# Kernel tuning notes

Hardware: AMD Instinct MI355X
Metric: run time of the kernel (lower is better)

The kernel has to match this reference:

```python
import jax, jax.numpy as jnp
import numpy as np

B, N, D_POINTS, D_MODEL = 2, 2048, 32, 512


def _gather(feat, idx):
    # feat: [B, N, C], idx: [B, N, K] -> [B, N, K, C]
    return jax.vmap(lambda f, i: f[i])(feat, idx)


def setup_inputs() -> dict:
    key = jax.random.key(0)
    ks = jax.random.split(key, 20)
    def lin(k, fan_in, fan_out):
        bound = 1.0 / np.sqrt(fan_in)
        return jax.random.uniform(k, (fan_in, fan_out), jnp.float32, -bound, bound)
    def bias(k, fan_in, fan_out):
        bound = 1.0 / np.sqrt(fan_in)
        return jax.random.uniform(k, (fan_out,), jnp.float32, -bound, bound)
    return {
        "xyz": jax.random.normal(ks[0], (B, N, 3), jnp.float32),
        "points": jax.random.normal(ks[1], (B, N, D_POINTS), jnp.float32),
        "fc1_w": lin(ks[2], D_POINTS, D_MODEL), "fc1_b": bias(ks[3], D_POINTS, D_MODEL),
        "fc2_w": lin(ks[4], D_MODEL, D_POINTS), "fc2_b": bias(ks[5], D_MODEL, D_POINTS),
        "delta_w1": lin(ks[6], 3, D_MODEL), "delta_b1": bias(ks[7], 3, D_MODEL),
        "delta_w2": lin(ks[8], D_MODEL, D_MODEL), "delta_b2": bias(ks[9], D_MODEL, D_MODEL),
        "gamma_w1": lin(ks[10], D_MODEL, D_MODEL), "gamma_b1": bias(ks[11], D_MODEL, D_MODEL),
        "gamma_w2": lin(ks[12], D_MODEL, D_MODEL), "gamma_b2": bias(ks[13], D_MODEL, D_MODEL),
        "wq": lin(ks[14], D_MODEL, D_MODEL),
        "wk": lin(ks[15], D_MODEL, D_MODEL),
        "wv": lin(ks[16], D_MODEL, D_MODEL),
        "knn_k": 16,
    }


def reference(xyz, points, fc1_w, fc1_b, fc2_w, fc2_b,
              delta_w1, delta_b1, delta_w2, delta_b2,
              gamma_w1, gamma_b1, gamma_w2, gamma_b2,
              wq, wk, wv, knn_k):
    # square_distance: [B, N, N]
    sq = jnp.sum(xyz * xyz, axis=-1)
    dists = sq[:, :, None] + sq[:, None, :] - 2.0 * jnp.einsum('bnc,bmc->bnm', xyz, xyz)
    # knn: k smallest distances (argsort[:, :, :k] equivalent)
    _, knn_idx = jax.lax.top_k(-dists, knn_k)           # [B, N, K]
    knn_xyz = _gather(xyz, knn_idx)                      # [B, N, K, 3]

    pre = points
    x = points @ fc1_w + fc1_b                           # [B, N, d_model]
    q = x @ wq                                           # [B, N, d_model]
    k = _gather(x @ wk, knn_idx)                         # [B, N, K, d_model]
    v = _gather(x @ wv, knn_idx)                         # [B, N, K, d_model]

    # positional encoding MLP on delta xyz
    delta = xyz[:, :, None, :] - knn_xyz                 # [B, N, K, 3]
    pos_enc = jax.nn.relu(delta @ delta_w1 + delta_b1) @ delta_w2 + delta_b2

    # gamma MLP on (q - k + pos_enc)
    a = q[:, :, None, :] - k + pos_enc
    a = jax.nn.relu(a @ gamma_w1 + gamma_b1) @ gamma_w2 + gamma_b2

    scale = jnp.asarray(np.sqrt(D_MODEL), a.dtype)
    attn = jax.nn.softmax(a / scale, axis=-2)            # softmax over neighbors, per channel

    res = jnp.sum(attn * (v + pos_enc), axis=2)          # einsum 'bmnf,bmnf->bmf'
    res = res @ fc2_w + fc2_b + pre                      # [B, N, d_points]
    return res, attn
```

## Files before the change

### kernel.cpp

```cpp
#include <hip/hip_runtime.h>
#include <hip/hip_bf16.h>
#include <math.h>

typedef __bf16 bf16_t;
typedef float f32x4 __attribute__((ext_vector_type(4)));
typedef bf16_t bf16x8 __attribute__((ext_vector_type(8)));

#define BM 128
#define BN 128
#define BKT 64
#define LDK 72

struct TC6 { const float* src[6]; bf16_t* dst[6]; };
__global__ __launch_bounds__(256) void tcast6_kernel(TC6 tc) {
  int job = blockIdx.x >> 10;
  int idx = (blockIdx.x & 1023) * 256 + threadIdx.x;
  int n = idx >> 9, k = idx & 511;
  tc.dst[job][idx] = (bf16_t)tc.src[job][k * 512 + n];
}

__global__ __launch_bounds__(256) void knn_kernel(const float* __restrict__ xyz, int* __restrict__ knn) {
  __shared__ float sx[2048], sy[2048], sz[2048], sq[2048];
  int tid = threadIdx.x;
  int lane = tid & 63, wave = tid >> 6;
  int gq = blockIdx.x * 4 + wave;
  int b  = gq >> 11;
  int base = b << 11;
  for (int p = tid; p < 2048; p += 256) {
    float x = xyz[(base + p) * 3 + 0];
    float y = xyz[(base + p) * 3 + 1];
    float z = xyz[(base + p) * 3 + 2];
    sx[p] = x; sy[p] = y; sz[p] = z;
    sq[p] = __fadd_rn(__fadd_rn(__fmul_rn(x, x), __fmul_rn(y, y)), __fmul_rn(z, z));
  }
  __syncthreads();
  int iq = gq & 2047;
  float qx = sx[iq], qy = sy[iq], qz = sz[iq], sqi = sq[iq];

  unsigned long long key[32];
  #pragma unroll
  for (int j = 0; j < 32; ++j) {
    int p = lane + j * 64;
    float d = __fmul_rn(sx[p], qx);
    d = fmaf(sy[p], qy, d);
    d = fmaf(sz[p], qz, d);
    float dist = __fsub_rn(__fadd_rn(sqi, sq[p]), __fmul_rn(2.0f, d));
    unsigned int bits = __float_as_uint(dist);
    unsigned int sk = bits ^ (unsigned int)(((int)bits >> 31) | 0x80000000);
    key[j] = ((unsigned long long)sk << 32) | (unsigned int)p;
  }

  int r = 0;
  #pragma unroll 1
  for (int s = 0; s < 16; ++s) {
    unsigned long long m = key[0];
    #pragma unroll
    for (int j = 1; j < 32; ++j) m = (key[j] < m) ? key[j] : m;
    #pragma unroll
    for (int off = 32; off > 0; off >>= 1) {
      unsigned long long o = (unsigned long long)__shfl_xor((long long)m, off);
      if (o < m) m = o;
    }
    if (lane == s) r = base + (int)(m & 0xFFFFFFFFu);
    #pragma unroll
    for (int j = 0; j < 32; ++j) key[j] = (key[j] == m) ? ~0ULL : key[j];
  }
  if (lane < 16) knn[gq * 16 + lane] = r;
}

__global__ __launch_bounds__(256) void xfeat_kernel(const float* __restrict__ points, const float* __restrict__ fc1_w,
                                                    const float* __restrict__ fc1_b, bf16_t* __restrict__ xb) {
  __shared__ float p[32];
  int m = blockIdx.x, tid = threadIdx.x;
  if (tid < 32) p[tid] = points[m * 32 + tid];
  __syncthreads();
  for (int c = tid; c < 512; c += 256) {
    float a = fc1_b[c];
    #pragma unroll
    for (int kk = 0; kk < 32; ++kk) a = fmaf(p[kk], fc1_w[kk * 512 + c], a);
    xb[m * 512 + c] = (bf16_t)a;
  }
}

__global__ __launch_bounds__(256) void h1_kernel(const float* __restrict__ xyz, const int* __restrict__ knn,
                                                 const float* __restrict__ dw1, const float* __restrict__ db1,
                                                 bf16_t* __restrict__ h1) {
  __shared__ float w0[512], w1r[512], w2[512], bb[512];
  int g = blockIdx.x, tid = threadIdx.x;
  for (int c = tid; c < 512; c += 256) {
    w0[c] = dw1[c]; w1r[c] = dw1[512 + c]; w2[c] = dw1[1024 + c]; bb[c] = db1[c];
  }
  float xi0 = xyz[g * 3 + 0], xi1 = xyz[g * 3 + 1], xi2 = xyz[g * 3 + 2];
  __syncthreads();
  for (int slot = 0; slot < 16; ++slot) {
    int j = knn[g * 16 + slot];
    float d0 = xi0 - xyz[j * 3 + 0];
    float d1 = xi1 - xyz[j * 3 + 1];
    float d2 = xi2 - xyz[j * 3 + 2];
    int m = g * 16 + slot;
    for (int c = tid; c < 512; c += 256) {
      float h = fmaf(d2, w2[c], fmaf(d1, w1r[c], d0 * w0[c])) + bb[c];
      h1[m * 512 + c] = (bf16_t)fmaxf(h, 0.0f);
    }
  }
}

__global__ __launch_bounds__(256) void final_kernel(const float* __restrict__ res_mid, const float* __restrict__ fc2_w,
                                                    const float* __restrict__ fc2_b, const float* __restrict__ points,
                                                    float* __restrict__ out) {
  int oid = blockIdx.x * 256 + threadIdx.x;
  int m = oid >> 5, c = oid & 31;
  float a = fc2_b[c];
  const float* rm = res_mid + m * 512;
  for (int kk = 0; kk < 512; ++kk) a = fmaf(rm[kk], fc2_w[kk * 32 + c], a);
  out[oid] = a + points[oid];
}

template <int SRC, int EPI>
__global__ __launch_bounds__(256) void gemm_kernel(
    const bf16_t* __restrict__ A, const bf16_t* __restrict__ Bt,
    float* __restrict__ Cf, bf16_t* __restrict__ Cb,
    const float* __restrict__ bias, int ldc,
    const float* __restrict__ qkv, float* pe_attn,
    const int* __restrict__ knn, float* __restrict__ res_mid)
{
  __shared__ bf16_t Alds[BM][LDK];
  __shared__ bf16_t Blds[BN][LDK];
  int tid  = threadIdx.x;
  int lane = tid & 63, wave = tid >> 6;
  int wr = wave >> 1, wc = wave & 1;
  int lr = lane & 15, lg = lane >> 4;
  int n0 = blockIdx.x * BN, m0 = blockIdx.y * BM;

  f32x4 acc[4][4];
  #pragma unroll
  for (int i = 0; i < 4; ++i)
    #pragma unroll
    for (int j = 0; j < 4; ++j) acc[i][j] = (f32x4){0.f, 0.f, 0.f, 0.f};

  int srow = tid >> 3;
  int sc8  = (tid & 7) * 8;

  for (int k0 = 0; k0 < 512; k0 += BKT) {
    #pragma unroll
    for (int it = 0; it < 4; ++it) {
      int r = srow + it * 32;
      if (SRC == 0) {
        bf16x8 v = *(const bf16x8*)(A + (size_t)(m0 + r) * 512 + k0 + sc8);
        *(bf16x8*)(&Alds[r][sc8]) = v;
      } else {
        int m = m0 + r;
        int g = m >> 4;
        int j = knn[m];
        const float* qp = qkv + (size_t)g * 1536 + k0 + sc8;
        const float* kp = qkv + (size_t)j * 1536 + 512 + k0 + sc8;
        const float* pp = pe_attn + (size_t)m * 512 + k0 + sc8;
        f32x4 q0 = *(const f32x4*)qp,       q1 = *(const f32x4*)(qp + 4);
        f32x4 k0v = *(const f32x4*)kp,      k1v = *(const f32x4*)(kp + 4);
        f32x4 p0 = *(const f32x4*)pp,       p1 = *(const f32x4*)(pp + 4);
        bf16x8 o;
        #pragma unroll
        for (int u = 0; u < 4; ++u) o[u] = (bf16_t)(q0[u] - k0v[u] + p0[u]);
        #pragma unroll
        for (int u = 0; u < 4; ++u) o[4 + u] = (bf16_t)(q1[u] - k1v[u] + p1[u]);
        *(bf16x8*)(&Alds[r][sc8]) = o;
      }
      bf16x8 vb = *(const bf16x8*)(Bt + (size_t)(n0 + r) * 512 + k0 + sc8);
      *(bf16x8*)(&Blds[r][sc8]) = vb;
    }
    __syncthreads();
    #pragma unroll
    for (int kk = 0; kk < BKT; kk += 32) {
      int ko = kk + 8 * lg;
      bf16x8 af[4], bfr[4];
      #pragma unroll
      for (int mi = 0; mi < 4; ++mi) af[mi] = *(const bf16x8*)(&Alds[wr * 64 + mi * 16 + lr][ko]);
      #pragma unroll
      for (int nj = 0; nj < 4; ++nj) bfr[nj] = *(const bf16x8*)(&Blds[wc * 64 + nj * 16 + lr][ko]);
      #pragma unroll
      for (int mi = 0; mi < 4; ++mi)
        #pragma unroll
        for (int nj = 0; nj < 4; ++nj)
          acc[mi][nj] = __builtin_amdgcn_mfma_f32_16x16x32_bf16(af[mi], bfr[nj], acc[mi][nj], 0, 0, 0);
    }
    __syncthreads();
  }

  if (EPI == 0 || EPI == 1) {
    #pragma unroll
    for (int mi = 0; mi < 4; ++mi)
      #pragma unroll
      for (int nj = 0; nj < 4; ++nj) {
        int col = n0 + wc * 64 + nj * 16 + lr;
        #pragma unroll
        for (int r = 0; r < 4; ++r) {
          int row = m0 + wr * 64 + mi * 16 + lg * 4 + r;
          float v = acc[mi][nj][r];
          if (EPI == 1) v += bias[col];
          Cf[(size_t)row * ldc + col] = v;
        }
      }
  } else if (EPI == 2) {
    #pragma unroll
    for (int mi = 0; mi < 4; ++mi)
      #pragma unroll
      for (int nj = 0; nj < 4; ++nj) {
        int col = n0 + wc * 64 + nj * 16 + lr;
        #pragma unroll
        for (int r = 0; r < 4; ++r) {
          int row = m0 + wr * 64 + mi * 16 + lg * 4 + r;
          Cb[(size_t)row * ldc + col] = (bf16_t)fmaxf(acc[mi][nj][r] + bias[col], 0.0f);
        }
      }
  } else {
    const float scale = 22.62741699796952f;
    #pragma unroll
    for (int mi = 0; mi < 4; ++mi) {
      int g = (m0 + wr * 64 + mi * 16) >> 4;
      #pragma unroll
      for (int nj = 0; nj < 4; ++nj) {
        int col = n0 + wc * 64 + nj * 16 + lr;
        float sv[4];
        float mx = -INFINITY;
        #pragma unroll
        for (int r = 0; r < 4; ++r) {
          sv[r] = (acc[mi][nj][r] + bias[col]) / scale;
          mx = fmaxf(mx, sv[r]);
        }
        mx = fmaxf(mx, __shfl_xor(mx, 16));
        mx = fmaxf(mx, __shfl_xor(mx, 32));
        float e[4], sum = 0.f;
        #pragma unroll
        for (int r = 0; r < 4; ++r) { e[r] = expf(sv[r] - mx); sum += e[r]; }
        sum += __shfl_xor(sum, 16);
        sum += __shfl_xor(sum, 32);
        float part = 0.f;
        #pragma unroll
        for (int r = 0; r < 4; ++r) {
          int row = g * 16 + lg * 4 + r;
          float at = e[r] / sum;
          int j = knn[row];
          float vv  = qkv[(size_t)j * 1536 + 1024 + col];
          float pev = pe_attn[(size_t)row * 512 + col];
          part = fmaf(at, vv + pev, part);
          pe_attn[(size_t)row * 512 + col] = at;
        }
        part += __shfl_xor(part, 16);
        part += __shfl_xor(part, 32);
        if (lg == 0) res_mid[(size_t)g * 512 + col] = part;
      }
    }
  }
}

extern "C" void kernel_launch(void* const* d_in, const int* in_sizes, int n_in,
                              void* d_out, int out_size, void* d_ws, size_t ws_size,
                              hipStream_t stream) {
  const float* xyz    = (const float*)d_in[0];
  const float* points = (const float*)d_in[1];
  const float* fc1_w  = (const float*)d_in[2];
  const float* fc1_b  = (const float*)d_in[3];
  const float* fc2_w  = (const float*)d_in[4];
  const float* fc2_b  = (const float*)d_in[5];
  const float* dw1    = (const float*)d_in[6];
  const float* db1    = (const float*)d_in[7];
  const float* dw2    = (const float*)d_in[8];
  const float* db2    = (const float*)d_in[9];
  const float* gw1    = (const float*)d_in[10];
  const float* gb1    = (const float*)d_in[11];
  const float* gw2    = (const float*)d_in[12];
  const float* gb2    = (const float*)d_in[13];
  const float* wq     = (const float*)d_in[14];
  const float* wk     = (const float*)d_in[15];
  const float* wv     = (const float*)d_in[16];

  float* out = (float*)d_out;
  float* attn_pe = out + 131072;

  char* w = (char*)d_ws;
  bf16_t* wqkvT  = (bf16_t*)w; w += (size_t)1536 * 512 * 2;
  bf16_t* dw2T   = (bf16_t*)w; w += (size_t)512 * 512 * 2;
  bf16_t* gw1T   = (bf16_t*)w; w += (size_t)512 * 512 * 2;
  bf16_t* gw2T   = (bf16_t*)w; w += (size_t)512 * 512 * 2;
  int*    knn    = (int*)w;    w += (size_t)65536 * 4;
  bf16_t* xb     = (bf16_t*)w; w += (size_t)4096 * 512 * 2;
  float*  qkv    = (float*)w;  w += (size_t)4096 * 1536 * 4;
  bf16_t* h12    = (bf16_t*)w; w += (size_t)65536 * 512 * 2;
  float*  res_mid= (float*)w;  w += (size_t)4096 * 512 * 4;

  TC6 tc;
  tc.src[0] = wq;  tc.dst[0] = wqkvT;
  tc.src[1] = wk;  tc.dst[1] = wqkvT + 512 * 512;
  tc.src[2] = wv;  tc.dst[2] = wqkvT + 2 * 512 * 512;
  tc.src[3] = dw2; tc.dst[3] = dw2T;
  tc.src[4] = gw1; tc.dst[4] = gw1T;
  tc.src[5] = gw2; tc.dst[5] = gw2T;
  tcast6_kernel<<<6144, 256, 0, stream>>>(tc);

  knn_kernel<<<1024, 256, 0, stream>>>(xyz, knn);
  xfeat_kernel<<<4096, 256, 0, stream>>>(points, fc1_w, fc1_b, xb);

  gemm_kernel<0, 0><<<dim3(12, 32), 256, 0, stream>>>(xb, wqkvT, qkv, nullptr, nullptr, 1536,
                                                      nullptr, nullptr, nullptr, nullptr);
  h1_kernel<<<4096, 256, 0, stream>>>(xyz, knn, dw1, db1, h12);

  gemm_kernel<0, 1><<<dim3(4, 512), 256, 0, stream>>>(h12, dw2T, attn_pe, nullptr, db2, 512,
                                                      nullptr, nullptr, nullptr, nullptr);

  gemm_kernel<1, 2><<<dim3(4, 512), 256, 0, stream>>>(nullptr, gw1T, nullptr, h12, gb1, 512,
                                                      qkv, attn_pe, knn, nullptr);

  gemm_kernel<0, 3><<<dim3(4, 512), 256, 0, stream>>>(h12, gw2T, nullptr, nullptr, gb2, 512,
                                                      qkv, attn_pe, knn, res_mid);

  final_kernel<<<512, 256, 0, stream>>>(res_mid, fc2_w, fc2_b, points, out);
}
```

Baseline: 468.1 us.

## Use direct global-to-LDS loads and XCD-aware block swizzle in GEMM

Replaces register-staged global loads of bf16 tiles with global_load_lds direct-to-LDS transfers for the B operand and the plain A operand. The LDS padding (LDK=72) is dropped to an unpadded layout that the direct loads require. Workgroup IDs are remapped so consecutive tiles land on the same XCD for L2 reuse. The unpadded layout risks LDS bank conflicts on the MFMA fragment reads, and the swizzle assumes the workgroup count is divisible by 8.

```diff
diff --git a/kernel.cpp b/kernel.cpp
--- a/kernel.cpp
+++ b/kernel.cpp
@@ -9,7 +9,10 @@
 #define BM 128
 #define BN 128
 #define BKT 64
-#define LDK 72
+
+#define GLD_LDS16(gp, lp) __builtin_amdgcn_global_load_lds( \
+    (const __attribute__((address_space(1))) void*)(gp), \
+    (__attribute__((address_space(3))) void*)(lp), 16, 0, 0)
 
 struct TC6 { const float* src[6]; bf16_t* dst[6]; };
 __global__ __launch_bounds__(256) void tcast6_kernel(TC6 tc) {
@@ -124,13 +127,21 @@
     const float* __restrict__ qkv, float* pe_attn,
     const int* __restrict__ knn, float* __restrict__ res_mid)
 {
-  __shared__ bf16_t Alds[BM][LDK];
-  __shared__ bf16_t Blds[BN][LDK];
+  __shared__ bf16_t Alds[BM * BKT];
+  __shared__ bf16_t Blds[BN * BKT];
   int tid  = threadIdx.x;
   int lane = tid & 63, wave = tid >> 6;
   int wr = wave >> 1, wc = wave & 1;
   int lr = lane & 15, lg = lane >> 4;
-  int n0 = blockIdx.x * BN, m0 = blockIdx.y * BM;
+
+  int gx = gridDim.x;
+  int nwg = gx * gridDim.y;
+  int orig = blockIdx.y * gx + blockIdx.x;
+  int cpx = nwg >> 3;
+  int swz = (orig & 7) * cpx + (orig >> 3);
+  int bx = swz % gx;
+  int by = swz / gx;
+  int n0 = bx * BN, m0 = by * BM;
 
   f32x4 acc[4][4];
   #pragma unroll
@@ -142,31 +153,37 @@
   int sc8  = (tid & 7) * 8;
 
   for (int k0 = 0; k0 < 512; k0 += BKT) {
-    #pragma unroll
-    for (int it = 0; it < 4; ++it) {
-      int r = srow + it * 32;
-      if (SRC == 0) {
-        bf16x8 v = *(const bf16x8*)(A + (size_t)(m0 + r) * 512 + k0 + sc8);
-        *(bf16x8*)(&Alds[r][sc8]) = v;
-      } else {
+    if (SRC == 0) {
+      #pragma unroll
+      for (int it = 0; it < 4; ++it) {
+        int r = it * 32 + srow;
+        GLD_LDS16(A + (size_t)(m0 + r) * 512 + k0 + sc8, Alds + (it * 4 + wave) * 512);
+      }
+    } else {
+      #pragma unroll
+      for (int it = 0; it < 4; ++it) {
+        int r = it * 32 + srow;
         int m = m0 + r;
         int g = m >> 4;
         int j = knn[m];
         const float* qp = qkv + (size_t)g * 1536 + k0 + sc8;
         const float* kp = qkv + (size_t)j * 1536 + 512 + k0 + sc8;
         const float* pp = pe_attn + (size_t)m * 512 + k0 + sc8;
-        f32x4 q0 = *(const f32x4*)qp,       q1 = *(const f32x4*)(qp + 4);
-        f32x4 k0v = *(const f32x4*)kp,      k1v = *(const f32x4*)(kp + 4);
-        f32x4 p0 = *(const f32x4*)pp,       p1 = *(const f32x4*)(pp + 4);
+        f32x4 q0 = *(const f32x4*)qp,  q1 = *(const f32x4*)(qp + 4);
+        f32x4 k0v = *(const f32x4*)kp, k1v = *(const f32x4*)(kp + 4);
+        f32x4 p0 = *(const f32x4*)pp,  p1 = *(const f32x4*)(pp + 4);
         bf16x8 o;
         #pragma unroll
         for (int u = 0; u < 4; ++u) o[u] = (bf16_t)(q0[u] - k0v[u] + p0[u]);
         #pragma unroll
         for (int u = 0; u < 4; ++u) o[4 + u] = (bf16_t)(q1[u] - k1v[u] + p1[u]);
-        *(bf16x8*)(&Alds[r][sc8]) = o;
-      }
-      bf16x8 vb = *(const bf16x8*)(Bt + (size_t)(n0 + r) * 512 + k0 + sc8);
-      *(bf16x8*)(&Blds[r][sc8]) = vb;
+        *(bf16x8*)(&Alds[r * BKT + sc8]) = o;
+      }
+    }
+    #pragma unroll
+    for (int it = 0; it < 4; ++it) {
+      int r = it * 32 + srow;
+      GLD_LDS16(Bt + (size_t)(n0 + r) * 512 + k0 + sc8, Blds + (it * 4 + wave) * 512);
     }
     __syncthreads();
     #pragma unroll
@@ -174,9 +191,9 @@
       int ko = kk + 8 * lg;
       bf16x8 af[4], bfr[4];
       #pragma unroll
-      for (int mi = 0; mi < 4; ++mi) af[mi] = *(const bf16x8*)(&Alds[wr * 64 + mi * 16 + lr][ko]);
-      #pragma unroll
-      for (int nj = 0; nj < 4; ++nj) bfr[nj] = *(const bf16x8*)(&Blds[wc * 64 + nj * 16 + lr][ko]);
+      for (int mi = 0; mi < 4; ++mi) af[mi] = *(const bf16x8*)(&Alds[(wr * 64 + mi * 16 + lr) * BKT + ko]);
+      #pragma unroll
+      for (int nj = 0; nj < 4; ++nj) bfr[nj] = *(const bf16x8*)(&Blds[(wc * 64 + nj * 16 + lr) * BKT + ko]);
       #pragma unroll
       for (int mi = 0; mi < 4; ++mi)
         #pragma unroll
```

After: 432.9 us. -7.5%, faster.
